# Optimization experiments

Measured on AMD Instinct MI355X. Metric: run time of the kernel, lower is better.

The kernel has to match this reference:

```python
import jax, jax.numpy as jnp
import numpy as np

SFREQ = 200.0
PATCH = 60
STRIDE = 30           # patch_size * (1 - overlap)
NPERSEG = min(PATCH // 2, 32)   # = 30
STEP = NPERSEG // 2   # scipy welch default noverlap = nperseg//2
NSEG = (PATCH - NPERSEG) // STEP + 1
NF = NPERSEG // 2 + 1
_w = 0.5 * (1.0 - np.cos(2.0 * np.pi * np.arange(NPERSEG) / NPERSEG))  # periodic hann (scipy default)
HANN = jnp.asarray(_w, jnp.float32)
WIN_NORM = float(SFREQ * np.sum(_w ** 2))  # density scaling
_f = np.arange(NF) * SFREQ / NPERSEG
FREQS = jnp.asarray(_f, jnp.float32)
BANDS = jnp.asarray(np.stack([((_f >= lo) & (_f <= hi)).astype(np.float32)
                              for lo, hi in [(1, 4), (4, 8), (8, 13), (13, 30), (30, 99)]]), jnp.float32)
ONESIDED = jnp.asarray(np.concatenate([[1.0], 2.0 * np.ones(NF - 2), [1.0]]), jnp.float32)


def layer_norm(v, g, b, eps=1e-5):
    mu = v.mean(-1, keepdims=True)
    var = ((v - mu) ** 2).mean(-1, keepdims=True)
    return (v - mu) * jax.lax.rsqrt(var + eps) * g + b


def features(p):
    # p: (B, P, PATCH)
    L = p.shape[-1]
    mx = p.max(-1); mn = p.min(-1); mean = p.mean(-1)
    c = p - mean[..., None]
    m2 = (c ** 2).mean(-1); m3 = (c ** 3).mean(-1); m4 = (c ** 4).mean(-1)
    std = jnp.sqrt(m2)
    peak_loc = jnp.argmax(jnp.abs(p), -1).astype(jnp.float32) / L
    dx = jnp.diff(p, axis=-1)
    zc = jnp.sum(jnp.diff(jnp.sign(p + 1e-10), axis=-1) != 0, axis=-1).astype(jnp.float32) / L
    kurt = m4 / (m2 ** 2) - 3.0   # scipy Fisher, biased
    skew = m3 / (m2 ** 1.5)
    morph = jnp.stack([mx, mn, mx - mn, mean, std, peak_loc,
                       dx.max(-1), dx.min(-1), jnp.abs(dx).mean(-1),
                       zc, (p ** 2).sum(-1), kurt, skew], -1)
    morph = jnp.where(jnp.isfinite(morph), morph, 0.0)
    # Welch PSD (detrend='constant', hann, density, one-sided, mean over segments)
    seg_idx = jnp.arange(NSEG)[:, None] * STEP + jnp.arange(NPERSEG)
    segs = p[..., seg_idx]                             # (B,P,NSEG,NPERSEG)
    segs = (segs - segs.mean(-1, keepdims=True)) * HANN
    X = jnp.fft.rfft(segs, axis=-1)                    # (B,P,NSEG,NF)
    psd = ((X.real ** 2 + X.imag ** 2) / WIN_NORM * ONESIDED).mean(-2)  # (B,P,NF)
    total = psd.sum(-1) + 1e-12
    bandp = jnp.einsum('bpf,kf->bpk', psd, BANDS) / total[..., None]
    peakf = FREQS[jnp.argmax(psd, -1)]
    cs = jnp.cumsum(psd, -1)
    edge = FREQS[jnp.argmax(cs >= 0.95 * total[..., None], -1)]
    pn = psd / total[..., None]
    ent = -jnp.sum(pn * jnp.log2(pn + 1e-12), -1)
    spec = jnp.concatenate([bandp, jnp.stack([peakf, edge, ent, total], -1)], -1)
    spec = jnp.where(jnp.isfinite(spec), spec, 0.0)
    return morph, spec


def setup_inputs() -> dict:
    key = jax.random.key(0)
    ks = jax.random.split(key, 8)
    B, T, E = 1024, 6000, 256
    n_m, n_s = 13, 9
    nf = n_m + n_s
    x = jax.random.normal(ks[0], (B, 1, T), jnp.float32)
    return {
        'x': x,
        'g_m': jnp.ones((n_m,), jnp.float32), 'b_m': jnp.zeros((n_m,), jnp.float32),
        'g_s': jnp.ones((n_s,), jnp.float32), 'b_s': jnp.zeros((n_s,), jnp.float32),
        'W1': jax.random.normal(ks[1], (nf, E // 2), jnp.float32) * 0.05,
        'b1': jnp.zeros((E // 2,), jnp.float32),
        'W2': jax.random.normal(ks[2], (E // 2, E), jnp.float32) * 0.05,
        'b2': jnp.zeros((E,), jnp.float32),
        'g_o': jnp.ones((E,), jnp.float32), 'b_o': jnp.zeros((E,), jnp.float32),
    }


def reference(x, g_m, b_m, g_s, b_s, W1, b1, W2, b2, g_o, b_o):
    B, _, T = x.shape
    n_patches = (T - PATCH) // STRIDE + 1
    idx = jnp.arange(n_patches)[:, None] * STRIDE + jnp.arange(PATCH)
    p = x[:, 0, :][:, idx]                     # (B, n_patches, PATCH)
    morph, spec = features(p)
    combined = jnp.concatenate([layer_norm(morph, g_m, b_m), layer_norm(spec, g_s, b_s)], -1)
    h = jax.nn.gelu(combined @ W1 + b1, approximate=False)  # dropout = identity (eval)
    return layer_norm(h @ W2 + b2, g_o, b_o)   # (B, n_patches, emb_size)
```

## Files before the change

### kernel.cpp

```cpp
#include <hip/hip_runtime.h>
#include <math.h>

#define NPERSEG 30
#define STEPW 15
#define NSEG 3
#define NF 16
#define PATCH 60
#define STRIDE 30
#define NP_ROW 199
#define NBATCH 1024
#define T_LEN 6000
#define NPATCH_TOTAL (NBATCH * NP_ROW)
#define GB 32
#define NBLK_B (NPATCH_TOTAL / GB)

constexpr double TC[30] = {
  1.0,
  0.97814760073380563793,
  0.91354545764260089550,
  0.80901699437494742410,
  0.66913060635885821383,
  0.5,
  0.30901699437494742410,
  0.10452846326765347140,
 -0.10452846326765347140,
 -0.30901699437494742410,
 -0.5,
 -0.66913060635885821383,
 -0.80901699437494742410,
 -0.91354545764260089550,
 -0.97814760073380563793,
 -1.0,
 -0.97814760073380563793,
 -0.91354545764260089550,
 -0.80901699437494742410,
 -0.66913060635885821383,
 -0.5,
 -0.30901699437494742410,
 -0.10452846326765347140,
  0.10452846326765347140,
  0.30901699437494742410,
  0.5,
  0.66913060635885821383,
  0.80901699437494742410,
  0.91354545764260089550,
  0.97814760073380563793,
};
constexpr double TS[30] = {
  0.0,
  0.20791169081775933710,
  0.40673664307580020775,
  0.58778525229247312917,
  0.74314482547739423501,
  0.86602540378443864676,
  0.95105651629515357212,
  0.99452189536827333692,
  0.99452189536827333692,
  0.95105651629515357212,
  0.86602540378443864676,
  0.74314482547739423501,
  0.58778525229247312917,
  0.40673664307580020775,
  0.20791169081775933710,
  0.0,
 -0.20791169081775933710,
 -0.40673664307580020775,
 -0.58778525229247312917,
 -0.74314482547739423501,
 -0.86602540378443864676,
 -0.95105651629515357212,
 -0.99452189536827333692,
 -0.99452189536827333692,
 -0.95105651629515357212,
 -0.86602540378443864676,
 -0.74314482547739423501,
 -0.58778525229247312917,
 -0.40673664307580020775,
 -0.20791169081775933710,
};
constexpr double INV_WN = 1.0 / 2250.0;
constexpr double THIRD  = 1.0 / 3.0;

__device__ __forceinline__ float np_sum30_f32(const float* a) {
    float r[8];
#pragma unroll
    for (int j = 0; j < 8; ++j) r[j] = a[j];
#pragma unroll
    for (int i = 8; i < 24; i += 8)
#pragma unroll
        for (int j = 0; j < 8; ++j) r[j] += a[i + j];
    float res = ((r[0] + r[1]) + (r[2] + r[3])) + ((r[4] + r[5]) + (r[6] + r[7]));
#pragma unroll
    for (int i = 24; i < 30; ++i) res += a[i];
    return res;
}

__device__ __forceinline__ double np_sum16_f64(const double* a) {
    double r[8];
#pragma unroll
    for (int j = 0; j < 8; ++j) r[j] = a[j] + a[8 + j];
    return ((r[0] + r[1]) + (r[2] + r[3])) + ((r[4] + r[5]) + (r[6] + r[7]));
}

__global__ __launch_bounds__(256) void feat_kernel(
    const float* __restrict__ x,
    const float* __restrict__ g_m, const float* __restrict__ b_m,
    const float* __restrict__ g_s, const float* __restrict__ b_s,
    float* __restrict__ out)
{
    __shared__ float xs[T_LEN];

    const int tid = threadIdx.x;
    const int row = blockIdx.x;

    {
        const float4* src = reinterpret_cast<const float4*>(x + (size_t)row * T_LEN);
        float4* dst = reinterpret_cast<float4*>(xs);
        for (int i = tid; i < T_LEN / 4; i += 256) dst[i] = src[i];
    }
    __syncthreads();
    if (tid >= NP_ROW) return;

    const float* pf = xs + tid * STRIDE;
    const int p = row * NP_ROW + tid;
    float* op = out + (size_t)(p >> 5) * (GB * 256) + (size_t)(p & 31) * 22;

    double morph[13];
    {
        const float v0f = pf[0];
        const double v0 = (double)v0f;
        double vmax = v0, vmin = v0, vsum = v0;
        float aval = fabsf(v0f); int amax = 0;
        float sv0 = v0f + 1e-10f;
        int prev = (sv0 > 0.0f) - (sv0 < 0.0f);
        int zc = 0;
        double dmax = 0.0, dmin = 0.0, dabssum = 0.0;
        double vprev = v0;
#pragma unroll
        for (int n = 1; n < PATCH; ++n) {
            const float vf = pf[n];
            const double v = (double)vf;
            vmax = fmax(vmax, v); vmin = fmin(vmin, v); vsum += v;
            const float a = fabsf(vf);
            if (a > aval) { aval = a; amax = n; }
            const float sv = vf + 1e-10f;
            const int sg = (sv > 0.0f) - (sv < 0.0f);
            if (sg != prev) zc++;
            prev = sg;
            const double d = v - vprev;
            if (n == 1) { dmax = d; dmin = d; dabssum = fabs(d); }
            else { dmax = fmax(dmax, d); dmin = fmin(dmin, d); dabssum += fabs(d); }
            vprev = v;
        }
        const double vmean = vsum / 60.0;
        const double dabsmean = dabssum / 59.0;
        const double peak_loc = (double)((float)amax / 60.0f);
        const double zcf = (double)zc / 60.0;

        double s2 = 0.0, s3 = 0.0, s4 = 0.0, ssq = 0.0;
#pragma unroll
        for (int n = 0; n < PATCH; ++n) {
            const double v = (double)pf[n];
            const double c = v - vmean, c2 = c * c;
            s2 += c2; s3 += c2 * c; s4 += c2 * c2;
            ssq += v * v;
        }
        const double m2 = s2 / 60.0, m3 = s3 / 60.0, m4 = s4 / 60.0;
        const double vstd = sqrt(m2);
        const double kurt = m4 / (m2 * m2) - 3.0;
        const double skew = m3 / (m2 * sqrt(m2));

        morph[0] = vmax;  morph[1] = vmin;  morph[2] = vmax - vmin;
        morph[3] = vmean; morph[4] = vstd;  morph[5] = peak_loc;
        morph[6] = dmax;  morph[7] = dmin;  morph[8] = dabsmean;
        morph[9] = zcf;   morph[10] = ssq;  morph[11] = kurt; morph[12] = skew;
#pragma unroll
        for (int i = 0; i < 13; ++i) if (!isfinite(morph[i])) morph[i] = 0.0;
    }
    {
        double mu = 0.0;
#pragma unroll
        for (int i = 0; i < 13; ++i) mu += morph[i];
        mu /= 13.0;
        double var = 0.0;
#pragma unroll
        for (int i = 0; i < 13; ++i) { double d = morph[i] - mu; var += d * d; }
        var /= 13.0;
        const double inv = 1.0 / sqrt(var + 1e-5);
        float fm[13];
#pragma unroll
        for (int i = 0; i < 13; ++i)
            fm[i] = (float)((morph[i] - mu) * inv * (double)g_m[i] + (double)b_m[i]);
#pragma unroll
        for (int i = 0; i < 6; ++i)
            *reinterpret_cast<float2*>(op + 2 * i) = make_float2(fm[2 * i], fm[2 * i + 1]);
        op[12] = fm[12];
    }

    asm volatile("" ::: "memory");

    double psd[NF];
#pragma unroll
    for (int k = 0; k < NF; ++k) psd[k] = 0.0;

#pragma unroll 1
    for (int s = 0; s < NSEG; ++s) {
        float y[NPERSEG];
        {
            float q[NPERSEG];
#pragma unroll
            for (int n = 0; n < NPERSEG; ++n) q[n] = pf[s * STEPW + n];
            const float res = np_sum30_f32(q);
            const float smean = res / 30.0f;
#pragma unroll
            for (int n = 0; n < NPERSEG; ++n) {
                const float hn = (float)(0.5 * (1.0 - TC[n]));
                y[n] = (q[n] - smean) * hn;
            }
        }
        const double y0d  = (double)y[0];
        const double y15d = (double)y[15];

        {
            double re[8], im[8];
#pragma unroll
            for (int j = 0; j < 8; ++j) {
                re[j] = (j & 1) ? (y0d - y15d) : (y0d + y15d);
                im[j] = 0.0;
            }
#pragma unroll
            for (int m = 1; m < 15; ++m) {
                const double u = (double)y[m] + (double)y[NPERSEG - m];
                const double v = (double)y[m] - (double)y[NPERSEG - m];
#pragma unroll
                for (int j = 0; j < 8; ++j) {
                    const double tcv = TC[(j * m) % 30];
                    const double tsv = TS[(j * m) % 30];
                    re[j] += u * tcv;
                    if (tsv != 0.0) im[j] += v * tsv;
                }
            }
#pragma unroll
            for (int j = 0; j < 8; ++j) {
                double pw = re[j] * re[j] + im[j] * im[j];
                pw *= INV_WN;
                if (j != 0) pw = pw + pw;
                psd[j] += pw;
            }
        }
        {
            double re[8], im[8];
#pragma unroll
            for (int j = 0; j < 8; ++j) {
                re[j] = (j & 1) ? (y0d - y15d) : (y0d + y15d);
                im[j] = 0.0;
            }
#pragma unroll
            for (int m = 1; m < 15; ++m) {
                const double u = (double)y[m] + (double)y[NPERSEG - m];
                const double v = (double)y[m] - (double)y[NPERSEG - m];
#pragma unroll
                for (int j = 0; j < 8; ++j) {
                    const int k = 8 + j;
                    const double tcv = TC[(k * m) % 30];
                    const double tsv = TS[(k * m) % 30];
                    re[j] += u * tcv;
                    if (tsv != 0.0) im[j] += v * tsv;
                }
            }
#pragma unroll
            for (int j = 0; j < 8; ++j) {
                double pw = re[j] * re[j] + im[j] * im[j];
                pw *= INV_WN;
                if (j != 7) pw = pw + pw;
                psd[8 + j] += pw;
            }
        }
    }
#pragma unroll
    for (int k = 0; k < NF; ++k) psd[k] = psd[k] * THIRD;

    const double total = np_sum16_f64(psd) + 1e-12;
    const double invt = 1.0 / total;

    const double band1 = psd[1] * invt;
    const double band3 = ((psd[2] + psd[3]) + psd[4]) * invt;
    double b4s = 0.0;
#pragma unroll
    for (int k = 5; k <= 14; ++k) b4s += psd[k];
    const double band4 = b4s * invt;

    int bk = 0; double bpv = psd[0];
#pragma unroll
    for (int k = 1; k < NF; ++k) if (psd[k] > bpv) { bpv = psd[k]; bk = k; }

    const double th = 0.95 * total;
    int ek = 0;
    {
        double acc = 0.0; bool found = false;
#pragma unroll
        for (int k = 0; k < NF; ++k) {
            acc += psd[k];
            if (!found && acc >= th) { ek = k; found = true; }
        }
    }

    double ent = 0.0;
#pragma unroll
    for (int k = 0; k < NF; ++k) {
        const double pn = psd[k] * invt;
        ent -= pn * log2(pn + 1e-12);
    }

    double spec[9];
    spec[0] = 0.0;
    spec[1] = band1;
    spec[2] = 0.0;
    spec[3] = band3;
    spec[4] = band4;
    spec[5] = (double)((float)((double)bk * 200.0 / 30.0));
    spec[6] = (double)((float)((double)ek * 200.0 / 30.0));
    spec[7] = ent;
    spec[8] = total;
#pragma unroll
    for (int i = 0; i < 9; ++i) if (!isfinite(spec[i])) spec[i] = 0.0;

    {
        double mu = 0.0;
#pragma unroll
        for (int i = 0; i < 9; ++i) mu += spec[i];
        mu /= 9.0;
        double var = 0.0;
#pragma unroll
        for (int i = 0; i < 9; ++i) { double d = spec[i] - mu; var += d * d; }
        var /= 9.0;
        const double inv = 1.0 / sqrt(var + 1e-5);
        float fs[9];
#pragma unroll
        for (int i = 0; i < 9; ++i)
            fs[i] = (float)((spec[i] - mu) * inv * (double)g_s[i] + (double)b_s[i]);
        op[13] = fs[0];
#pragma unroll
        for (int i = 0; i < 4; ++i)
            *reinterpret_cast<float2*>(op + 14 + 2 * i) = make_float2(fs[1 + 2 * i], fs[2 + 2 * i]);
    }
}

__global__ __launch_bounds__(256, 8) void mlp_kernel(
    const float* __restrict__ W1, const float* __restrict__ b1,
    const float* __restrict__ W2, const float* __restrict__ b2,
    const float* __restrict__ g_o, const float* __restrict__ b_o,
    float* __restrict__ out)
{
    __shared__ float Fsl[GB * 22];
    __shared__ float Hs[GB][128];

    const int tid = threadIdx.x;
    const size_t base = (size_t)blockIdx.x * (GB * 256);

    if (tid < 176)
        reinterpret_cast<float4*>(Fsl)[tid] =
            *reinterpret_cast<const float4*>(out + base + 4 * (size_t)tid);
    __syncthreads();

    {
        const int hc  = tid & 127;
        const int ppb = tid >> 7;
        float w1c[22];
#pragma unroll
        for (int k = 0; k < 22; ++k) w1c[k] = W1[k * 128 + hc];
        const float b1v = b1[hc];
#pragma unroll
        for (int v = 0; v < 16; ++v) {
            const int pp = ppb + 2 * v;
            float a = b1v;
#pragma unroll
            for (int k = 0; k < 22; ++k) a += Fsl[pp * 22 + k] * w1c[k];
            Hs[pp][hc] = 0.5f * a * (1.0f + erff(a * 0.70710678118654752440f));
        }
    }
    __syncthreads();

    const int cb = tid & 63;
    const int wv = tid >> 6;

    float4 acc[8];
    {
        const float4 b2v = *reinterpret_cast<const float4*>(b2 + 4 * cb);
#pragma unroll
        for (int p = 0; p < 8; ++p) acc[p] = b2v;
    }

#pragma unroll 2
    for (int k = 0; k < 128; k += 4) {
        float4 w0 = *reinterpret_cast<const float4*>(&W2[(k + 0) * 256 + 4 * cb]);
        float4 w1 = *reinterpret_cast<const float4*>(&W2[(k + 1) * 256 + 4 * cb]);
        float4 w2 = *reinterpret_cast<const float4*>(&W2[(k + 2) * 256 + 4 * cb]);
        float4 w3 = *reinterpret_cast<const float4*>(&W2[(k + 3) * 256 + 4 * cb]);
#pragma unroll
        for (int p = 0; p < 8; ++p) {
            const float4 h = *reinterpret_cast<const float4*>(&Hs[8 * wv + p][k]);
            acc[p].x += h.x * w0.x; acc[p].y += h.x * w0.y;
            acc[p].z += h.x * w0.z; acc[p].w += h.x * w0.w;
            acc[p].x += h.y * w1.x; acc[p].y += h.y * w1.y;
            acc[p].z += h.y * w1.z; acc[p].w += h.y * w1.w;
            acc[p].x += h.z * w2.x; acc[p].y += h.z * w2.y;
            acc[p].z += h.z * w2.z; acc[p].w += h.z * w2.w;
            acc[p].x += h.w * w3.x; acc[p].y += h.w * w3.y;
            acc[p].z += h.w * w3.z; acc[p].w += h.w * w3.w;
        }
    }

    const float4 go4 = *reinterpret_cast<const float4*>(g_o + 4 * cb);
    const float4 bo4 = *reinterpret_cast<const float4*>(b_o + 4 * cb);
#pragma unroll
    for (int p = 0; p < 8; ++p) {
        float s = (acc[p].x + acc[p].y) + (acc[p].z + acc[p].w);
        float q = (acc[p].x * acc[p].x + acc[p].y * acc[p].y)
                + (acc[p].z * acc[p].z + acc[p].w * acc[p].w);
        for (int off = 32; off; off >>= 1) {
            s += __shfl_xor(s, off);
            q += __shfl_xor(q, off);
        }
        const float mu  = s * (1.0f / 256.0f);
        const float var = q * (1.0f / 256.0f) - mu * mu;
        const float inv = rsqrtf(var + 1e-5f);
        float4 o;
        o.x = (acc[p].x - mu) * inv * go4.x + bo4.x;
        o.y = (acc[p].y - mu) * inv * go4.y + bo4.y;
        o.z = (acc[p].z - mu) * inv * go4.z + bo4.z;
        o.w = (acc[p].w - mu) * inv * go4.w + bo4.w;
        *reinterpret_cast<float4*>(out + base + (size_t)(8 * wv + p) * 256 + 4 * cb) = o;
    }
}

extern "C" void kernel_launch(void* const* d_in, const int* in_sizes, int n_in,
                              void* d_out, int out_size, void* d_ws, size_t ws_size,
                              hipStream_t stream) {
    const float* x   = (const float*)d_in[0];
    const float* g_m = (const float*)d_in[1];
    const float* b_m = (const float*)d_in[2];
    const float* g_s = (const float*)d_in[3];
    const float* b_s = (const float*)d_in[4];
    const float* W1  = (const float*)d_in[5];
    const float* b1  = (const float*)d_in[6];
    const float* W2  = (const float*)d_in[7];
    const float* b2  = (const float*)d_in[8];
    const float* g_o = (const float*)d_in[9];
    const float* b_o = (const float*)d_in[10];
    float* out = (float*)d_out;

    feat_kernel<<<NBATCH, 256, 0, stream>>>(x, g_m, b_m, g_s, b_s, out);
    mlp_kernel<<<NBLK_B, 256, 0, stream>>>(W1, b1, W2, b2, g_o, b_o, out);
}
```

Baseline: 443.7 us.

## Split per-patch DFT halves across two thread groups in feature kernel

The feature kernel now launches 512 threads per row, and two threads work on each patch. Each thread computes one half of the DFT frequency bins, and the halves are exchanged through shared memory. The second thread also computes the morphological features while the first does the spectral post-processing. The goal is to cut the long serial double-precision work per thread and give the GPU more waves to hide latency, at the cost of an extra barrier, extra LDS, and recomputing the segment windowing in both threads. The MLP launch-bounds occupancy hint also drops from 8 to 6.

```diff
diff --git a/kernel.cpp b/kernel.cpp
--- a/kernel.cpp
+++ b/kernel.cpp
@@ -102,13 +102,65 @@
     return ((r[0] + r[1]) + (r[2] + r[3])) + ((r[4] + r[5]) + (r[6] + r[7]));
 }
 
-__global__ __launch_bounds__(256) void feat_kernel(
+template<int KBASE>
+__device__ __forceinline__ void dft_half(const float* __restrict__ pf, double* psdh) {
+#pragma unroll
+    for (int j = 0; j < 8; ++j) psdh[j] = 0.0;
+#pragma unroll 1
+    for (int s = 0; s < NSEG; ++s) {
+        float y[NPERSEG];
+        {
+            float q[NPERSEG];
+#pragma unroll
+            for (int n = 0; n < NPERSEG; ++n) q[n] = pf[s * STEPW + n];
+            const float res = np_sum30_f32(q);
+            const float smean = res / 30.0f;
+#pragma unroll
+            for (int n = 0; n < NPERSEG; ++n) {
+                const float hn = (float)(0.5 * (1.0 - TC[n]));
+                y[n] = (q[n] - smean) * hn;
+            }
+        }
+        const double y0d  = (double)y[0];
+        const double y15d = (double)y[15];
+        double re[8], im[8];
+#pragma unroll
+        for (int j = 0; j < 8; ++j) {
+            re[j] = ((KBASE + j) & 1) ? (y0d - y15d) : (y0d + y15d);
+            im[j] = 0.0;
+        }
+#pragma unroll
+        for (int m = 1; m < 15; ++m) {
+            const double u = (double)y[m] + (double)y[NPERSEG - m];
+            const double v = (double)y[m] - (double)y[NPERSEG - m];
+#pragma unroll
+            for (int j = 0; j < 8; ++j) {
+                const double tcv = TC[((KBASE + j) * m) % 30];
+                const double tsv = TS[((KBASE + j) * m) % 30];
+                re[j] += u * tcv;
+                if (tsv != 0.0) im[j] += v * tsv;
+            }
+        }
+#pragma unroll
+        for (int j = 0; j < 8; ++j) {
+            double pw = re[j] * re[j] + im[j] * im[j];
+            pw *= INV_WN;
+            if ((KBASE + j) != 0 && (KBASE + j) != NF - 1) pw = pw + pw;
+            psdh[j] += pw;
+        }
+    }
+#pragma unroll
+    for (int j = 0; j < 8; ++j) psdh[j] *= THIRD;
+}
+
+__global__ __launch_bounds__(512) void feat_kernel(
     const float* __restrict__ x,
     const float* __restrict__ g_m, const float* __restrict__ b_m,
     const float* __restrict__ g_s, const float* __restrict__ b_s,
     float* __restrict__ out)
 {
-    __shared__ float xs[T_LEN];
+    __shared__ float  xs[T_LEN];
+    __shared__ double psd1s[NP_ROW][9];
 
     const int tid = threadIdx.x;
     const int row = blockIdx.x;
@@ -116,237 +168,179 @@
     {
         const float4* src = reinterpret_cast<const float4*>(x + (size_t)row * T_LEN);
         float4* dst = reinterpret_cast<float4*>(xs);
-        for (int i = tid; i < T_LEN / 4; i += 256) dst[i] = src[i];
+        for (int i = tid; i < T_LEN / 4; i += 512) dst[i] = src[i];
     }
     __syncthreads();
-    if (tid >= NP_ROW) return;
-
-    const float* pf = xs + tid * STRIDE;
-    const int p = row * NP_ROW + tid;
+
+    const int pid  = tid & 255;
+    const int role = tid >> 8;
+    const bool active = pid < NP_ROW;
+
+    const float* pf = xs + pid * STRIDE;
+    const int p = row * NP_ROW + pid;
     float* op = out + (size_t)(p >> 5) * (GB * 256) + (size_t)(p & 31) * 22;
 
-    double morph[13];
-    {
-        const float v0f = pf[0];
-        const double v0 = (double)v0f;
-        double vmax = v0, vmin = v0, vsum = v0;
-        float aval = fabsf(v0f); int amax = 0;
-        float sv0 = v0f + 1e-10f;
-        int prev = (sv0 > 0.0f) - (sv0 < 0.0f);
-        int zc = 0;
-        double dmax = 0.0, dmin = 0.0, dabssum = 0.0;
-        double vprev = v0;
-#pragma unroll
-        for (int n = 1; n < PATCH; ++n) {
-            const float vf = pf[n];
-            const double v = (double)vf;
-            vmax = fmax(vmax, v); vmin = fmin(vmin, v); vsum += v;
-            const float a = fabsf(vf);
-            if (a > aval) { aval = a; amax = n; }
-            const float sv = vf + 1e-10f;
-            const int sg = (sv > 0.0f) - (sv < 0.0f);
-            if (sg != prev) zc++;
-            prev = sg;
-            const double d = v - vprev;
-            if (n == 1) { dmax = d; dmin = d; dabssum = fabs(d); }
-            else { dmax = fmax(dmax, d); dmin = fmin(dmin, d); dabssum += fabs(d); }
-            vprev = v;
-        }
-        const double vmean = vsum / 60.0;
-        const double dabsmean = dabssum / 59.0;
-        const double peak_loc = (double)((float)amax / 60.0f);
-        const double zcf = (double)zc / 60.0;
-
-        double s2 = 0.0, s3 = 0.0, s4 = 0.0, ssq = 0.0;
-#pragma unroll
-        for (int n = 0; n < PATCH; ++n) {
-            const double v = (double)pf[n];
-            const double c = v - vmean, c2 = c * c;
-            s2 += c2; s3 += c2 * c; s4 += c2 * c2;
-            ssq += v * v;
-        }
-        const double m2 = s2 / 60.0, m3 = s3 / 60.0, m4 = s4 / 60.0;
-        const double vstd = sqrt(m2);
-        const double kurt = m4 / (m2 * m2) - 3.0;
-        const double skew = m3 / (m2 * sqrt(m2));
-
-        morph[0] = vmax;  morph[1] = vmin;  morph[2] = vmax - vmin;
-        morph[3] = vmean; morph[4] = vstd;  morph[5] = peak_loc;
-        morph[6] = dmax;  morph[7] = dmin;  morph[8] = dabsmean;
-        morph[9] = zcf;   morph[10] = ssq;  morph[11] = kurt; morph[12] = skew;
-#pragma unroll
-        for (int i = 0; i < 13; ++i) if (!isfinite(morph[i])) morph[i] = 0.0;
-    }
-    {
-        double mu = 0.0;
-#pragma unroll
-        for (int i = 0; i < 13; ++i) mu += morph[i];
-        mu /= 13.0;
-        double var = 0.0;
-#pragma unroll
-        for (int i = 0; i < 13; ++i) { double d = morph[i] - mu; var += d * d; }
-        var /= 13.0;
-        const double inv = 1.0 / sqrt(var + 1e-5);
-        float fm[13];
-#pragma unroll
-        for (int i = 0; i < 13; ++i)
-            fm[i] = (float)((morph[i] - mu) * inv * (double)g_m[i] + (double)b_m[i]);
-#pragma unroll
-        for (int i = 0; i < 6; ++i)
-            *reinterpret_cast<float2*>(op + 2 * i) = make_float2(fm[2 * i], fm[2 * i + 1]);
-        op[12] = fm[12];
-    }
-
-    asm volatile("" ::: "memory");
-
-    double psd[NF];
-#pragma unroll
-    for (int k = 0; k < NF; ++k) psd[k] = 0.0;
-
-#pragma unroll 1
-    for (int s = 0; s < NSEG; ++s) {
-        float y[NPERSEG];
+    double psdh[8];
+    if (active) {
+        if (role == 0) {
+            dft_half<0>(pf, psdh);
+        } else {
+            dft_half<8>(pf, psdh);
+#pragma unroll
+            for (int j = 0; j < 8; ++j) psd1s[pid][j] = psdh[j];
+        }
+    }
+    __syncthreads();
+
+    if (active && role == 1) {
+        double morph[13];
         {
-            float q[NPERSEG];
-#pragma unroll
-            for (int n = 0; n < NPERSEG; ++n) q[n] = pf[s * STEPW + n];
-            const float res = np_sum30_f32(q);
-            const float smean = res / 30.0f;
-#pragma unroll
-            for (int n = 0; n < NPERSEG; ++n) {
-                const float hn = (float)(0.5 * (1.0 - TC[n]));
-                y[n] = (q[n] - smean) * hn;
+            const float v0f = pf[0];
+            const double v0 = (double)v0f;
+            double vmax = v0, vmin = v0, vsum = v0;
+            float aval = fabsf(v0f); int amax = 0;
+            float sv0 = v0f + 1e-10f;
+            int prev = (sv0 > 0.0f) - (sv0 < 0.0f);
+            int zc = 0;
+            double dmax = 0.0, dmin = 0.0, dabssum = 0.0;
+            double vprev = v0;
+#pragma unroll
+            for (int n = 1; n < PATCH; ++n) {
+                const float vf = pf[n];
+                const double v = (double)vf;
+                vmax = fmax(vmax, v); vmin = fmin(vmin, v); vsum += v;
+                const float a = fabsf(vf);
+                if (a > aval) { aval = a; amax = n; }
+                const float sv = vf + 1e-10f;
+                const int sg = (sv > 0.0f) - (sv < 0.0f);
+                if (sg != prev) zc++;
+                prev = sg;
+                const double d = v - vprev;
+                if (n == 1) { dmax = d; dmin = d; dabssum = fabs(d); }
+                else { dmax = fmax(dmax, d); dmin = fmin(dmin, d); dabssum += fabs(d); }
+                vprev = v;
             }
-        }
-        const double y0d  = (double)y[0];
-        const double y15d = (double)y[15];
-
+            const double vmean = vsum / 60.0;
+            const double dabsmean = dabssum / 59.0;
+            const double peak_loc = (double)((float)amax / 60.0f);
+            const double zcf = (double)zc / 60.0;
+
+            double s2 = 0.0, s3 = 0.0, s4 = 0.0, ssq = 0.0;
+#pragma unroll
+            for (int n = 0; n < PATCH; ++n) {
+                const double v = (double)pf[n];
+                const double c = v - vmean, c2 = c * c;
+                s2 += c2; s3 += c2 * c; s4 += c2 * c2;
+                ssq += v * v;
+            }
+            const double m2 = s2 / 60.0, m3 = s3 / 60.0, m4 = s4 / 60.0;
+            const double vstd = sqrt(m2);
+            const double kurt = m4 / (m2 * m2) - 3.0;
+            const double skew = m3 / (m2 * sqrt(m2));
+
+            morph[0] = vmax;  morph[1] = vmin;  morph[2] = vmax - vmin;
+            morph[3] = vmean; morph[4] = vstd;  morph[5] = peak_loc;
+            morph[6] = dmax;  morph[7] = dmin;  morph[8] = dabsmean;
+            morph[9] = zcf;   morph[10] = ssq;  morph[11] = kurt; morph[12] = skew;
+#pragma unroll
+            for (int i = 0; i < 13; ++i) if (!isfinite(morph[i])) morph[i] = 0.0;
+        }
         {
-            double re[8], im[8];
-#pragma unroll
-            for (int j = 0; j < 8; ++j) {
-                re[j] = (j & 1) ? (y0d - y15d) : (y0d + y15d);
-                im[j] = 0.0;
+            double mu = 0.0;
+#pragma unroll
+            for (int i = 0; i < 13; ++i) mu += morph[i];
+            mu /= 13.0;
+            double var = 0.0;
+#pragma unroll
+            for (int i = 0; i < 13; ++i) { double d = morph[i] - mu; var += d * d; }
+            var /= 13.0;
+            const double inv = 1.0 / sqrt(var + 1e-5);
+            float fm[13];
+#pragma unroll
+            for (int i = 0; i < 13; ++i)
+                fm[i] = (float)((morph[i] - mu) * inv * (double)g_m[i] + (double)b_m[i]);
+#pragma unroll
+            for (int i = 0; i < 6; ++i)
+                *reinterpret_cast<float2*>(op + 2 * i) = make_float2(fm[2 * i], fm[2 * i + 1]);
+            op[12] = fm[12];
+        }
+    }
+
+    if (active && role == 0) {
+        double psd[NF];
+#pragma unroll
+        for (int j = 0; j < 8; ++j) psd[j] = psdh[j];
+#pragma unroll
+        for (int j = 0; j < 8; ++j) psd[8 + j] = psd1s[pid][j];
+
+        const double total = np_sum16_f64(psd) + 1e-12;
+        const double invt = 1.0 / total;
+
+        const double band1 = psd[1] * invt;
+        const double band3 = ((psd[2] + psd[3]) + psd[4]) * invt;
+        double b4s = 0.0;
+#pragma unroll
+        for (int k = 5; k <= 14; ++k) b4s += psd[k];
+        const double band4 = b4s * invt;
+
+        int bk = 0; double bpv = psd[0];
+#pragma unroll
+        for (int k = 1; k < NF; ++k) if (psd[k] > bpv) { bpv = psd[k]; bk = k; }
+
+        const double th = 0.95 * total;
+        int ek = 0;
+        {
+            double acc = 0.0; bool found = false;
+#pragma unroll
+            for (int k = 0; k < NF; ++k) {
+                acc += psd[k];
+                if (!found && acc >= th) { ek = k; found = true; }
             }
-#pragma unroll
-            for (int m = 1; m < 15; ++m) {
-                const double u = (double)y[m] + (double)y[NPERSEG - m];
-                const double v = (double)y[m] - (double)y[NPERSEG - m];
-#pragma unroll
-                for (int j = 0; j < 8; ++j) {
-                    const double tcv = TC[(j * m) % 30];
-                    const double tsv = TS[(j * m) % 30];
-                    re[j] += u * tcv;
-                    if (tsv != 0.0) im[j] += v * tsv;
-                }
-            }
-#pragma unroll
-            for (int j = 0; j < 8; ++j) {
-                double pw = re[j] * re[j] + im[j] * im[j];
-                pw *= INV_WN;
-                if (j != 0) pw = pw + pw;
-                psd[j] += pw;
-            }
-        }
+        }
+
+        double ent = 0.0;
+#pragma unroll
+        for (int k = 0; k < NF; ++k) {
+            const double pn = psd[k] * invt;
+            ent -= pn * log2(pn + 1e-12);
+        }
+
+        double spec[9];
+        spec[0] = 0.0;
+        spec[1] = band1;
+        spec[2] = 0.0;
+        spec[3] = band3;
+        spec[4] = band4;
+        spec[5] = (double)((float)((double)bk * 200.0 / 30.0));
+        spec[6] = (double)((float)((double)ek * 200.0 / 30.0));
+        spec[7] = ent;
+        spec[8] = total;
+#pragma unroll
+        for (int i = 0; i < 9; ++i) if (!isfinite(spec[i])) spec[i] = 0.0;
+
         {
-            double re[8], im[8];
-#pragma unroll
-            for (int j = 0; j < 8; ++j) {
-                re[j] = (j & 1) ? (y0d - y15d) : (y0d + y15d);
-                im[j] = 0.0;
-            }
-#pragma unroll
-            for (int m = 1; m < 15; ++m) {
-                const double u = (double)y[m] + (double)y[NPERSEG - m];
-                const double v = (double)y[m] - (double)y[NPERSEG - m];
-#pragma unroll
-                for (int j = 0; j < 8; ++j) {
-                    const int k = 8 + j;
-                    const double tcv = TC[(k * m) % 30];
-                    const double tsv = TS[(k * m) % 30];
-                    re[j] += u * tcv;
-                    if (tsv != 0.0) im[j] += v * tsv;
-                }
-            }
-#pragma unroll
-            for (int j = 0; j < 8; ++j) {
-                double pw = re[j] * re[j] + im[j] * im[j];
-                pw *= INV_WN;
-                if (j != 7) pw = pw + pw;
-                psd[8 + j] += pw;
-            }
-        }
-    }
-#pragma unroll
-    for (int k = 0; k < NF; ++k) psd[k] = psd[k] * THIRD;
-
-    const double total = np_sum16_f64(psd) + 1e-12;
-    const double invt = 1.0 / total;
-
-    const double band1 = psd[1] * invt;
-    const double band3 = ((psd[2] + psd[3]) + psd[4]) * invt;
-    double b4s = 0.0;
-#pragma unroll
-    for (int k = 5; k <= 14; ++k) b4s += psd[k];
-    const double band4 = b4s * invt;
-
-    int bk = 0; double bpv = psd[0];
-#pragma unroll
-    for (int k = 1; k < NF; ++k) if (psd[k] > bpv) { bpv = psd[k]; bk = k; }
-
-    const double th = 0.95 * total;
-    int ek = 0;
-    {
-        double acc = 0.0; bool found = false;
-#pragma unroll
-        for (int k = 0; k < NF; ++k) {
-            acc += psd[k];
-            if (!found && acc >= th) { ek = k; found = true; }
-        }
-    }
-
-    double ent = 0.0;
-#pragma unroll
-    for (int k = 0; k < NF; ++k) {
-        const double pn = psd[k] * invt;
-        ent -= pn * log2(pn + 1e-12);
-    }
-
-    double spec[9];
-    spec[0] = 0.0;
-    spec[1] = band1;
-    spec[2] = 0.0;
-    spec[3] = band3;
-    spec[4] = band4;
-    spec[5] = (double)((float)((double)bk * 200.0 / 30.0));
-    spec[6] = (double)((float)((double)ek * 200.0 / 30.0));
-    spec[7] = ent;
-    spec[8] = total;
-#pragma unroll
-    for (int i = 0; i < 9; ++i) if (!isfinite(spec[i])) spec[i] = 0.0;
-
-    {
-        double mu = 0.0;
-#pragma unroll
-        for (int i = 0; i < 9; ++i) mu += spec[i];
-        mu /= 9.0;
-        double var = 0.0;
-#pragma unroll
-        for (int i = 0; i < 9; ++i) { double d = spec[i] - mu; var += d * d; }
-        var /= 9.0;
-        const double inv = 1.0 / sqrt(var + 1e-5);
-        float fs[9];
-#pragma unroll
-        for (int i = 0; i < 9; ++i)
-            fs[i] = (float)((spec[i] - mu) * inv * (double)g_s[i] + (double)b_s[i]);
-        op[13] = fs[0];
-#pragma unroll
-        for (int i = 0; i < 4; ++i)
-            *reinterpret_cast<float2*>(op + 14 + 2 * i) = make_float2(fs[1 + 2 * i], fs[2 + 2 * i]);
-    }
-}
-
-__global__ __launch_bounds__(256, 8) void mlp_kernel(
+            double mu = 0.0;
+#pragma unroll
+            for (int i = 0; i < 9; ++i) mu += spec[i];
+            mu /= 9.0;
+            double var = 0.0;
+#pragma unroll
+            for (int i = 0; i < 9; ++i) { double d = spec[i] - mu; var += d * d; }
+            var /= 9.0;
+            const double inv = 1.0 / sqrt(var + 1e-5);
+            float fs[9];
+#pragma unroll
+            for (int i = 0; i < 9; ++i)
+                fs[i] = (float)((spec[i] - mu) * inv * (double)g_s[i] + (double)b_s[i]);
+            op[13] = fs[0];
+#pragma unroll
+            for (int i = 0; i < 4; ++i)
+                *reinterpret_cast<float2*>(op + 14 + 2 * i) = make_float2(fs[1 + 2 * i], fs[2 + 2 * i]);
+        }
+    }
+}
+
+__global__ __launch_bounds__(256, 6) void mlp_kernel(
     const float* __restrict__ W1, const float* __restrict__ b1,
     const float* __restrict__ W2, const float* __restrict__ b2,
     const float* __restrict__ g_o, const float* __restrict__ b_o,
@@ -450,6 +444,6 @@
     const float* b_o = (const float*)d_in[10];
     float* out = (float*)d_out;
 
-    feat_kernel<<<NBATCH, 256, 0, stream>>>(x, g_m, b_m, g_s, b_s, out);
+    feat_kernel<<<NBATCH, 512, 0, stream>>>(x, g_m, b_m, g_s, b_s, out);
     mlp_kernel<<<NBLK_B, 256, 0, stream>>>(W1, b1, W2, b2, g_o, b_o, out);
 }
```

New measurement: 456.7 us. 2.9% more time.
